# Kernel optimization log

Hardware: AMD Instinct MI355X
Metric: run time of the kernel (lower is better)

## Reference

```python
import jax, jax.numpy as jnp
import numpy as np

# Geometry constants hardcoded in the torch module
B, H, W = 1, 256, 256
A, DC = 64, 1024            # n_views, det_count
NSAMP = 512                  # samples per ray for the line integral
DSRC, DDET, SPACING = 500.0, 500.0, 2.0
NPAD = 2048                  # fft padding (next pow2 >= 2*DC)
FEAT = 32


def _bilinear_image(img, px, py):
    """Bilinear sample img (B,H,W) at centered coords px,py (any shape). Zero outside."""
    b, hh, ww = img.shape
    cx = px + (ww - 1) / 2.0
    cy = py + (hh - 1) / 2.0
    x0 = jnp.floor(cx); y0 = jnp.floor(cy)
    fx = cx - x0; fy = cy - y0
    x0i = x0.astype(jnp.int32); y0i = y0.astype(jnp.int32)
    flat = img.reshape(b, -1)

    def gather(yi, xi):
        valid = (yi >= 0) & (yi < hh) & (xi >= 0) & (xi < ww)
        yc = jnp.clip(yi, 0, hh - 1); xc = jnp.clip(xi, 0, ww - 1)
        idx = (yc * ww + xc).reshape(-1)
        v = jnp.take(flat, idx, axis=1).reshape((b,) + yi.shape)
        return v * valid.astype(img.dtype)

    return (gather(y0i, x0i) * (1 - fx) * (1 - fy)
            + gather(y0i, x0i + 1) * fx * (1 - fy)
            + gather(y0i + 1, x0i) * (1 - fx) * fy
            + gather(y0i + 1, x0i + 1) * fx * fy)


def fan_forward(img, theta):
    """Ray-driven fan-beam forward projection. img (B,1,H,W) -> sino (B,A,DC)."""
    im = img[:, 0]
    c = jnp.cos(theta); s = jnp.sin(theta)
    src = DSRC * jnp.stack([c, s], -1)                    # (A,2) source positions
    e = jnp.stack([-s, c], -1)                            # detector axis
    u = (jnp.arange(DC) - (DC - 1) / 2.0) * SPACING       # detector offsets
    det = -DDET * jnp.stack([c, s], -1)[:, None, :] + u[None, :, None] * e[:, None, :]  # (A,DC,2)
    d = det - src[:, None, :]
    L = jnp.sqrt(jnp.sum(d * d, axis=-1))                 # (A,DC) ray lengths
    t = (jnp.arange(NSAMP, dtype=jnp.float32) + 0.5) / NSAMP
    pts = src[:, None, None, :] + t[None, None, :, None] * d[:, :, None, :]  # (A,DC,N,2)
    vals = _bilinear_image(im, pts[..., 0], pts[..., 1])  # (B,A,DC,N)
    return jnp.sum(vals, axis=-1) * (L / NSAMP)[None]


def filter_sinogram(sino):
    """Ram-Lak ramp filtering along the detector axis with zero-padding."""
    f = jnp.abs(jnp.fft.rfftfreq(NPAD)).astype(jnp.float32)  # cycles/sample
    sf = jnp.fft.rfft(sino, n=NPAD, axis=-1) * (2.0 * f)
    return jnp.fft.irfft(sf, n=NPAD, axis=-1)[..., :DC].astype(sino.dtype)


def fan_backprojection(sino, theta):
    """Pixel-driven fan-beam backprojection. sino (B,A,DC) -> (B,1,H,W)."""
    xs = jnp.arange(W, dtype=jnp.float32) - (W - 1) / 2.0
    ys = jnp.arange(H, dtype=jnp.float32) - (H - 1) / 2.0
    gx, gy = jnp.meshgrid(xs, ys)                         # (H,W)
    c = jnp.cos(theta)[:, None, None]; s = jnp.sin(theta)[:, None, None]
    xr = gx[None] * c + gy[None] * s                      # (A,H,W) rotated coords
    yr = -gx[None] * s + gy[None] * c
    denom = DSRC - xr
    uu = yr * (DSRC + DDET) / denom                       # detector coordinate
    wgt = (DSRC * DSRC) / (denom * denom)                 # fan-beam distance weight
    iu = uu / SPACING + (DC - 1) / 2.0
    i0 = jnp.floor(iu); fr = iu - i0
    i0i = i0.astype(jnp.int32)
    aidx = jnp.arange(A)[:, None, None]
    b = sino.shape[0]
    flat = sino.reshape(b, -1)

    def g(ii):
        valid = (ii >= 0) & (ii < DC)
        ic = jnp.clip(ii, 0, DC - 1)
        idx = (aidx * DC + ic).reshape(-1)
        v = jnp.take(flat, idx, axis=1).reshape((b, A, H, W))
        return v * valid.astype(sino.dtype)

    vals = g(i0i) * (1 - fr) + g(i0i + 1) * fr            # (B,A,H,W)
    bp = jnp.sum(vals * wgt[None], axis=1) * (jnp.pi / A)
    return bp[:, None]


def conv(x, w):
    return jax.lax.conv_general_dilated(x, w, (1, 1), 'SAME',
                                        dimension_numbers=('NCHW', 'OIHW', 'NCHW'))


def setup_inputs():
    key = jax.random.key(0)
    ks = jax.random.split(key, 8)
    x = jax.random.normal(ks[0], (B, 1, H, W), jnp.float32)
    theta = jnp.arange(A, dtype=jnp.float32) * (2.0 * np.pi / A)
    sinogram = jax.random.normal(ks[1], (B, A, DC), jnp.float32)

    def xav(k, shape):
        fan_in = shape[1] * 9; fan_out = shape[0] * 9
        return jax.random.normal(k, shape, jnp.float32) * np.sqrt(2.0 / (fan_in + fan_out)).astype(np.float32)

    return {
        'x': x, 'theta': theta, 'sinogram': sinogram,
        'lambda_step': jnp.float32(0.5), 'soft_thr': jnp.float32(0.01),
        'conv1_forward': xav(ks[2], (FEAT, 1, 3, 3)),
        'conv2_forward': xav(ks[3], (FEAT, FEAT, 3, 3)),
        'conv1_backward': xav(ks[4], (FEAT, FEAT, 3, 3)),
        'conv2_backward': xav(ks[5], (1, FEAT, 3, 3)),
    }


def reference(x, theta, sinogram, lambda_step, soft_thr,
              conv1_forward, conv2_forward, conv1_backward, conv2_backward):
    sino_pred = fan_forward(x, theta)
    filtered = filter_sinogram(sino_pred)
    X_fbp = fan_backprojection(filtered - sinogram, theta)
    x_input = x - lambda_step * X_fbp
    h = jax.nn.relu(conv(x_input, conv1_forward))
    x_forward = conv(h, conv2_forward)
    hs = jnp.sign(x_forward) * jax.nn.relu(jnp.abs(x_forward) - soft_thr)
    x_pred = conv(jax.nn.relu(conv(hs, conv1_backward)), conv2_backward)
    x_est = conv(jax.nn.relu(conv(x_forward, conv1_backward)), conv2_backward)
    symloss = x_est - x_input
    return (x_pred, symloss)
```

## Files before the change

### kernel.cpp

```cpp
#include <hip/hip_runtime.h>

#define DEV_INLINE __device__ __forceinline__

#define PI_F 3.14159265358979323846f

#define H_OFF     0
#define SINO_OFF  2048
#define DIFF_OFF  67584
#define XIN_OFF   133120
#define WF2F_OFF  198656
#define WF1B_OFF  207872
#define WF2B_OFF  212480
#define BUFA_OFF  217088
#define BUFB_OFF  2314240

typedef short bf16x8 __attribute__((ext_vector_type(8)));
typedef float f32x4 __attribute__((ext_vector_type(4)));

union FragI4 { int4 i4; bf16x8 v; };
union I4U    { int4 i4; int i[4]; };

DEV_INLINE unsigned rne1(float a) {
  unsigned u = __float_as_uint(a);
  return (u + 0x7FFFu + ((u >> 16) & 1u)) >> 16;
}
DEV_INLINE int pack_rne(float a, float b) {
  return (int)(rne1(a) | (rne1(b) << 16));
}

__global__ __launch_bounds__(256) void setup_kernel(
    const float* __restrict__ sino_in, const float* __restrict__ w2f,
    const float* __restrict__ w1b, const float* __restrict__ w2b,
    const float* __restrict__ img,
    float* __restrict__ h, float* __restrict__ diff,
    int* __restrict__ wf2f, int* __restrict__ wf1b, int* __restrict__ wf2b,
    float4* __restrict__ quadP, float* __restrict__ x_input) {
  const int b = blockIdx.x;
  const int tid = threadIdx.x;
  if (b < 64) {
    __shared__ float hp[8][32];
    const int cell = tid & 31;
    const int kq = tid >> 5;
    const int n = b * 32 + cell;
    float ssum = 0.0f;
    const float ang_scale = PI_F / 1024.0f;
    for (int k = kq * 128; k < kq * 128 + 128; ++k) {
      int m = (k * n) & 2047;
      ssum += (float)k * __cosf((float)m * ang_scale);
    }
    hp[kq][cell] = ssum;
    __syncthreads();
    if (tid < 32) {
      float S = 0.0f;
      #pragma unroll
      for (int q = 0; q < 8; ++q) S += hp[q][tid];
      int nn = b * 32 + tid;
      float sgn = (nn & 1) ? -1.0f : 1.0f;
      h[nn] = (S * (1.0f / 512.0f) + sgn) * (1.0f / 2048.0f);
    }
  } else if (b < 320) {
    int idx = (b - 64) * 256 + tid;
    diff[idx] = -sino_in[idx];
  } else if (b < 356) {
    const bool second = (b >= 338);
    int idx = (b - (second ? 338 : 320)) * 256 + tid;
    int d = idx & 3;
    int L = (idx >> 2) & 63;
    int jm = idx >> 8;
    int j = jm >> 1, mt = jm & 1;
    int co = mt * 16 + (L & 15);
    int ci0 = (L >> 4) * 8 + 2 * d;
    const float* w = second ? w1b : w2f;
    int v = pack_rne(w[co * 288 + ci0 * 9 + j], w[co * 288 + (ci0 + 1) * 9 + j]);
    (second ? wf1b : wf2f)[idx] = v;
  } else if (b < 617) {
    int idx = (b - 356) * 256 + tid;
    if (idx < 258 * 258) {
      int y = idx / 258;
      int x = idx - y * 258;
      float4 v;
      int ay = y - 1, bx = x - 1;
      bool y0ok = (ay >= 0 && ay < 256);
      bool y1ok = (ay + 1 >= 0 && ay + 1 < 256);
      bool x0ok = (bx >= 0 && bx < 256);
      bool x1ok = (bx + 1 >= 0 && bx + 1 < 256);
      v.x = (y0ok && x0ok) ? img[(ay << 8) + bx] : 0.0f;
      v.y = (y0ok && x1ok) ? img[(ay << 8) + bx + 1] : 0.0f;
      v.z = (y1ok && x0ok) ? img[((ay + 1) << 8) + bx] : 0.0f;
      v.w = (y1ok && x1ok) ? img[((ay + 1) << 8) + bx + 1] : 0.0f;
      quadP[idx] = v;
    }
  } else if (b < 873) {
    int idx = (b - 617) * 256 + tid;
    x_input[idx] = img[idx];
  } else {
    int d = tid & 3;
    int L = tid >> 2;
    int n = L & 15;
    int k0 = (L >> 4) * 8 + 2 * d;
    float lo = (n < 9) ? w2b[k0 * 9 + n] : 0.0f;
    float hi = (n < 9) ? w2b[(k0 + 1) * 9 + n] : 0.0f;
    wf2b[tid] = pack_rne(lo, hi);
  }
}

__global__ __launch_bounds__(256) void fwdproj(
    const float4* __restrict__ quadP, const float* __restrict__ theta,
    float* __restrict__ sino) {
  __shared__ float part[8][32];
  __shared__ float cs[2];
  const int tid = threadIdx.x;
  const int a = blockIdx.x >> 5;
  const int cell = tid & 31;
  const int chunk = tid >> 5;
  const int d = ((blockIdx.x & 31) << 5) + cell;
  if (tid == 0) {
    float th = theta[a];
    cs[0] = cosf(th);
    cs[1] = sinf(th);
  }
  __syncthreads();
  const float c = cs[0], s = cs[1];
  const float u = ((float)d - 511.5f) * 2.0f;
  const float dxv = -1000.0f * c - u * s;
  const float dyv = -1000.0f * s + u * c;
  const float L = sqrtf(1.0e6f + u * u);
  const float sx = fmaf(500.0f, c, 127.5f);
  const float sy = fmaf(500.0f, s, 127.5f);

  float tlo = 0.0f, thi = 1.0f;
  if (fabsf(dxv) > 1e-6f) {
    float inv = 1.0f / dxv;
    float a0 = (-1.0f - sx) * inv, a1 = (256.0f - sx) * inv;
    tlo = fmaxf(tlo, fminf(a0, a1));
    thi = fminf(thi, fmaxf(a0, a1));
  } else if (sx <= -1.0f || sx >= 256.0f) {
    thi = -1.0f;
  }
  if (fabsf(dyv) > 1e-6f) {
    float inv = 1.0f / dyv;
    float a0 = (-1.0f - sy) * inv, a1 = (256.0f - sy) * inv;
    tlo = fmaxf(tlo, fminf(a0, a1));
    thi = fminf(thi, fmaxf(a0, a1));
  } else if (sy <= -1.0f || sy >= 256.0f) {
    thi = -1.0f;
  }
  int imin = (int)ceilf(tlo * 512.0f - 0.5f) - 1;
  imin = imin < 0 ? 0 : imin;
  int imax = (int)floorf(thi * 512.0f - 0.5f) + 1;
  imax = imax > 511 ? 511 : imax;

  float acc = 0.0f;
  for (int i = imin + chunk; i <= imax; i += 8) {
    float t = ((float)i + 0.5f) * (1.0f / 512.0f);
    float cx = fmaf(t, dxv, sx);
    float cy = fmaf(t, dyv, sy);
    cx = fminf(fmaxf(cx, -1.0f), 256.0f);
    cy = fminf(fmaxf(cy, -1.0f), 256.0f);
    float xf = floorf(cx), yf = floorf(cy);
    float fx = cx - xf, fy = cy - yf;
    int ix = (int)xf + 1;
    int iy = (int)yf + 1;
    float4 q = quadP[iy * 258 + ix];
    float gx = 1.0f - fx, gy = 1.0f - fy;
    acc += gy * (gx * q.x + fx * q.y) + fy * (gx * q.z + fx * q.w);
  }
  part[chunk][cell] = acc;
  __syncthreads();
  if (tid < 32) {
    float r = 0.0f;
    #pragma unroll
    for (int q = 0; q < 8; ++q) r += part[q][tid];
    sino[a * 1024 + ((blockIdx.x & 31) << 5) + tid] = r * (L * (1.0f / 512.0f));
  }
}

__global__ __launch_bounds__(256) void filt(
    const float* __restrict__ sino_pred, const float* __restrict__ h,
    float* __restrict__ diff) {
  __shared__ __align__(16) float srow[256];
  __shared__ __align__(16) float hext[4104];
  const int a = blockIdx.x >> 2;
  const int q = blockIdx.x & 3;
  const int tid = threadIdx.x;
  const int k0base = q * 256;
  srow[tid] = sino_pred[a * 1024 + k0base + tid];
  for (int n = tid; n < 4104; n += 256) hext[n] = h[(n - 2051) & 2047];
  __syncthreads();
  const int dd0 = tid * 4;
  float acc0 = 0.f, acc1 = 0.f, acc2 = 0.f, acc3 = 0.f;
  #pragma unroll 4
  for (int kk = 0; kk < 256; kk += 4) {
    float4 sv = *reinterpret_cast<const float4*>(&srow[kk]);
    int nb = dd0 + 2048 - k0base - kk;
    float4 hA = *reinterpret_cast<const float4*>(&hext[nb]);
    float4 hB = *reinterpret_cast<const float4*>(&hext[nb + 4]);
    acc0 = fmaf(sv.x, hA.w, acc0); acc0 = fmaf(sv.y, hA.z, acc0);
    acc0 = fmaf(sv.z, hA.y, acc0); acc0 = fmaf(sv.w, hA.x, acc0);
    acc1 = fmaf(sv.x, hB.x, acc1); acc1 = fmaf(sv.y, hA.w, acc1);
    acc1 = fmaf(sv.z, hA.z, acc1); acc1 = fmaf(sv.w, hA.y, acc1);
    acc2 = fmaf(sv.x, hB.y, acc2); acc2 = fmaf(sv.y, hB.x, acc2);
    acc2 = fmaf(sv.z, hA.w, acc2); acc2 = fmaf(sv.w, hA.z, acc2);
    acc3 = fmaf(sv.x, hB.z, acc3); acc3 = fmaf(sv.y, hB.y, acc3);
    acc3 = fmaf(sv.z, hB.x, acc3); acc3 = fmaf(sv.w, hA.w, acc3);
  }
  float* o = diff + a * 1024 + dd0;
  atomicAdd(o + 0, acc0);
  atomicAdd(o + 1, acc1);
  atomicAdd(o + 2, acc2);
  atomicAdd(o + 3, acc3);
}

__global__ __launch_bounds__(256) void backproj_part(
    const float* __restrict__ diff, const float* __restrict__ theta,
    const float* __restrict__ lam_p, float* __restrict__ x_input) {
  __shared__ float cst[16], snt[16];
  const int tid = threadIdx.x;
  const int tileb = blockIdx.x & 255;
  const int a0 = (blockIdx.x >> 8) << 4;
  if (tid < 16) {
    float th = theta[a0 + tid];
    cst[tid] = cosf(th);
    snt[tid] = sinf(th);
  }
  __syncthreads();
  const int tX = (tileb & 3) << 6;
  const int tY = (tileb >> 2) << 2;
  const int pxi = tX + (tid & 63);
  const int pyi = tY + (tid >> 6);
  const float gx = (float)pxi - 127.5f;
  const float gy = (float)pyi - 127.5f;
  float acc = 0.0f;
  for (int ai = 0; ai < 16; ++ai) {
    float c = cst[ai], s = snt[ai];
    float xr = gx * c + gy * s;
    float yr = gy * c - gx * s;
    float denom = 500.0f - xr;
    float inv = 1.0f / denom;
    float uu = yr * 1000.0f * inv;
    float wgt = 250000.0f * inv * inv;
    float iu = uu * 0.5f + 511.5f;
    float i0f = floorf(iu);
    float fr = iu - i0f;
    int i0 = (int)i0f;
    int c0 = min(max(i0, 0), 1023);
    int c1 = min(max(i0 + 1, 0), 1023);
    float m0 = (i0 >= 0 && i0 < 1024) ? 1.0f : 0.0f;
    float m1 = (i0 + 1 >= 0 && i0 + 1 < 1024) ? 1.0f : 0.0f;
    const float* row = diff + (a0 + ai) * 1024;
    float v0 = row[c0] * m0;
    float v1 = row[c1] * m1;
    acc += (v0 * (1.0f - fr) + v1 * fr) * wgt;
  }
  int p = (pyi << 8) + pxi;
  atomicAdd(x_input + p, -lam_p[0] * 0.04908738521234052f * acc);
}

__global__ __launch_bounds__(256) void conv12f(
    const float* __restrict__ x_input, const float* __restrict__ w1f,
    const int* __restrict__ wf2f, int* __restrict__ xfp) {
  __shared__ float xin[8][36];
  __shared__ __align__(16) int htile[3264];
  const int tid = threadIdx.x;
  const int lane = tid & 63;
  const int wave = tid >> 6;
  const int tX = (blockIdx.x & 7) << 5;
  const int tY = (blockIdx.x >> 3) << 2;

  FragI4 wf[2][9];
  const int4* wfg = (const int4*)wf2f;
  #pragma unroll
  for (int mt = 0; mt < 2; ++mt)
    #pragma unroll
    for (int j = 0; j < 9; ++j) wf[mt][j].i4 = wfg[(j * 2 + mt) * 64 + lane];

  for (int idx = tid; idx < 288; idx += 256) {
    int sy = idx / 36;
    int sx = idx - sy * 36;
    int gy = tY + sy - 2, gx = tX + sx - 2;
    xin[sy][sx] = (gy >= 0 && gy < 256 && gx >= 0 && gx < 256)
                      ? x_input[(gy << 8) + gx] : 0.0f;
  }
  __syncthreads();

  for (int pos = tid; pos < 204; pos += 256) {
    int yy = pos / 34;
    int xx = pos - yy * 34;
    int hy = tY + yy - 1, hx = tX + xx - 1;
    bool hin = (hy >= 0 && hy < 256 && hx >= 0 && hx < 256);
    float v[9];
    #pragma unroll
    for (int dy = 0; dy < 3; ++dy)
      #pragma unroll
      for (int dx = 0; dx < 3; ++dx) v[dy * 3 + dx] = xin[yy + dy][xx + dx];
    int packs[16];
    #pragma unroll
    for (int c2 = 0; c2 < 16; ++c2) {
      float r0 = 0.0f, r1 = 0.0f;
      #pragma unroll
      for (int j = 0; j < 9; ++j) {
        r0 = fmaf(v[j], w1f[(2 * c2) * 9 + j], r0);
        r1 = fmaf(v[j], w1f[(2 * c2 + 1) * 9 + j], r1);
      }
      r0 = hin ? fmaxf(r0, 0.0f) : 0.0f;
      r1 = hin ? fmaxf(r1, 0.0f) : 0.0f;
      packs[c2] = pack_rne(r0, r1);
    }
    #pragma unroll
    for (int g = 0; g < 4; ++g)
      *reinterpret_cast<int4*>(&htile[g * 816 + pos * 4]) =
          make_int4(packs[4 * g], packs[4 * g + 1],
                    packs[4 * g + 2], packs[4 * g + 3]);
  }
  __syncthreads();

  const int y = wave;
  const int n = lane & 15;
  const int q = lane >> 4;
  const int qb = q * 816;
  for (int xt = 0; xt < 2; ++xt) {
    const int x0 = xt << 4;
    f32x4 acc0 = {0.f, 0.f, 0.f, 0.f};
    f32x4 acc1 = {0.f, 0.f, 0.f, 0.f};
    #pragma unroll
    for (int j = 0; j < 9; ++j) {
      int dy = j / 3, dx = j - dy * 3;
      int pb = (y + dy) * 34 + x0 + dx + n;
      FragI4 bf;
      bf.i4 = *reinterpret_cast<const int4*>(&htile[qb + pb * 4]);
      acc0 = __builtin_amdgcn_mfma_f32_16x16x32_bf16(wf[0][j].v, bf.v, acc0, 0, 0, 0);
      acc1 = __builtin_amdgcn_mfma_f32_16x16x32_bf16(wf[1][j].v, bf.v, acc1, 0, 0, 0);
    }
    const int gpos = ((tY + y) << 8) + tX + x0 + n;
    int2* xp = (int2*)(xfp + (gpos << 4));
    xp[q]     = make_int2(pack_rne(acc0[0], acc0[1]), pack_rne(acc0[2], acc0[3]));
    xp[4 + q] = make_int2(pack_rne(acc1[0], acc1[1]), pack_rne(acc1[2], acc1[3]));
  }
}

__global__ __launch_bounds__(256) void branch_tail(
    const int* __restrict__ xfp, const int* __restrict__ wf1b,
    const int* __restrict__ wf2b, const float* __restrict__ thr_p,
    const float* __restrict__ x_input, float* __restrict__ out) {
  __shared__ __align__(16) int ldsX[8704];
  __shared__ __align__(16) int ldsD[6400];
  float* ldsP = (float*)ldsX;
  const int tid = threadIdx.x;
  const int lane = tid & 63;
  const int wave = tid >> 6;
  const int branch = blockIdx.x >> 8;
  const int tileb = blockIdx.x & 255;
  const int tX = (tileb & 3) << 6;
  const int tY = (tileb >> 2) << 2;
  const float thr = thr_p[0];
  const bool soft = (branch == 0);

  FragI4 wf[2][9];
  const int4* wfg = (const int4*)wf1b;
  #pragma unroll
  for (int mt = 0; mt < 2; ++mt)
    #pragma unroll
    for (int j = 0; j < 9; ++j) wf[mt][j].i4 = wfg[(j * 2 + mt) * 64 + lane];
  FragI4 wb;
  wb.i4 = ((const int4*)wf2b)[lane];

  if (tid < 16) {
    int g = tid >> 2, px = 396 + (tid & 3);
    *reinterpret_cast<int4*>(&ldsD[g * 1600 + px * 4]) = make_int4(0, 0, 0, 0);
  }

  #pragma unroll
  for (int t = 0; t < 3; ++t) {
    int p = tid + t * 256;
    if (p < 544) {
      int sy = p / 68;
      int sx = p - sy * 68;
      int gy = tY + sy - 2, gx = tX + sx - 2;
      bool ok = ((unsigned)gy < 256u) && ((unsigned)gx < 256u);
      I4U w[4];
      if (ok) {
        const int4* src = (const int4*)(xfp + (((gy << 8) + gx) << 4));
        w[0].i4 = src[0]; w[1].i4 = src[1]; w[2].i4 = src[2]; w[3].i4 = src[3];
      } else {
        w[0].i4 = w[1].i4 = w[2].i4 = w[3].i4 = make_int4(0, 0, 0, 0);
      }
      #pragma unroll
      for (int g = 0; g < 4; ++g) {
        if (soft) {
          #pragma unroll
          for (int k = 0; k < 4; ++k) {
            int v = w[g].i[k];
            float lo = __uint_as_float(((unsigned)v) << 16);
            float hi = __uint_as_float(((unsigned)v) & 0xFFFF0000u);
            lo = fmaxf(lo - thr, 0.0f) + fminf(lo + thr, 0.0f);
            hi = fmaxf(hi - thr, 0.0f) + fminf(hi + thr, 0.0f);
            w[g].i[k] = pack_rne(lo, hi);
          }
        }
        *reinterpret_cast<int4*>(&ldsX[g * 2176 + p * 4]) = w[g].i4;
      }
    }
  }
  __syncthreads();

  const int n = lane & 15;
  const int q = lane >> 4;
  const int rxtab[5] = {-1, 15, 31, 47, 49};
  for (int t = wave; t < 30; t += 4) {
    int trow = t / 5;
    int ry = trow - 1;
    int rx0 = rxtab[t - trow * 5];
    int rxn = rx0 + n;
    bool inimg = ((unsigned)(tX + rxn) < 256u) && ((unsigned)(tY + ry) < 256u);
    int pxD = (ry + 1) * 66 + rxn + 1;
    f32x4 acc0 = {0.f, 0.f, 0.f, 0.f};
    f32x4 acc1 = {0.f, 0.f, 0.f, 0.f};
    #pragma unroll
    for (int j = 0; j < 9; ++j) {
      int dy = j / 3, dx = j - dy * 3;
      int pb = (ry + 1 + dy) * 68 + rx0 + 1 + dx + n;
      FragI4 bf;
      bf.i4 = *reinterpret_cast<const int4*>(&ldsX[q * 2176 + pb * 4]);
      acc0 = __builtin_amdgcn_mfma_f32_16x16x32_bf16(wf[0][j].v, bf.v, acc0, 0, 0, 0);
      acc1 = __builtin_amdgcn_mfma_f32_16x16x32_bf16(wf[1][j].v, bf.v, acc1, 0, 0, 0);
    }
    float a00 = inimg ? fmaxf(acc0[0], 0.0f) : 0.0f;
    float a01 = inimg ? fmaxf(acc0[1], 0.0f) : 0.0f;
    float a02 = inimg ? fmaxf(acc0[2], 0.0f) : 0.0f;
    float a03 = inimg ? fmaxf(acc0[3], 0.0f) : 0.0f;
    float a10 = inimg ? fmaxf(acc1[0], 0.0f) : 0.0f;
    float a11 = inimg ? fmaxf(acc1[1], 0.0f) : 0.0f;
    float a12 = inimg ? fmaxf(acc1[2], 0.0f) : 0.0f;
    float a13 = inimg ? fmaxf(acc1[3], 0.0f) : 0.0f;
    *reinterpret_cast<int2*>(
        &ldsD[(q >> 1) * 1600 + pxD * 4 + (q & 1) * 2]) =
        make_int2(pack_rne(a00, a01), pack_rne(a02, a03));
    *reinterpret_cast<int2*>(
        &ldsD[(2 + (q >> 1)) * 1600 + pxD * 4 + (q & 1) * 2]) =
        make_int2(pack_rne(a10, a11), pack_rne(a12, a13));
  }
  __syncthreads();

  for (int t = wave; t < 25; t += 4) {
    int pbase = t << 4;
    FragI4 af;
    af.i4 = *reinterpret_cast<const int4*>(&ldsD[q * 1600 + (pbase + n) * 4]);
    f32x4 acc = {0.f, 0.f, 0.f, 0.f};
    acc = __builtin_amdgcn_mfma_f32_16x16x32_bf16(af.v, wb.v, acc, 0, 0, 0);
    #pragma unroll
    for (int r = 0; r < 4; ++r)
      ldsP[(pbase + q * 4 + r) * 17 + n] = acc[r];
  }
  __syncthreads();

  const int px = tid & 63, py = tid >> 6;
  float acc = 0.0f;
  #pragma unroll
  for (int j = 0; j < 9; ++j) {
    int dy = j / 3, dx = j - dy * 3;
    int rp = (py + dy) * 66 + px + dx;
    acc += ldsP[rp * 17 + j];
  }
  const int p = ((tY + py) << 8) + tX + px;
  if (branch == 0) out[p] = acc;
  else out[65536 + p] = acc - x_input[p];
}

extern "C" void kernel_launch(void* const* d_in, const int* in_sizes, int n_in,
                              void* d_out, int out_size, void* d_ws, size_t ws_size,
                              hipStream_t stream) {
  const float* x       = (const float*)d_in[0];
  const float* theta   = (const float*)d_in[1];
  const float* sino_in = (const float*)d_in[2];
  const float* lam     = (const float*)d_in[3];
  const float* thr     = (const float*)d_in[4];
  const float* w_c1f   = (const float*)d_in[5];
  const float* w_c2f   = (const float*)d_in[6];
  const float* w_c1b   = (const float*)d_in[7];
  const float* w_c2b   = (const float*)d_in[8];
  float* out = (float*)d_out;
  float* ws  = (float*)d_ws;

  float* h         = ws + H_OFF;
  float* sino_pred = ws + SINO_OFF;
  float* diff      = ws + DIFF_OFF;
  float* x_input   = ws + XIN_OFF;
  int*   wf2f      = (int*)(ws + WF2F_OFF);
  int*   wf1b      = (int*)(ws + WF1B_OFF);
  int*   wf2b      = (int*)(ws + WF2B_OFF);
  float4* quadP    = (float4*)(ws + BUFA_OFF);
  int*   xfp       = (int*)(ws + BUFB_OFF);

  setup_kernel<<<874, 256, 0, stream>>>(sino_in, w_c2f, w_c1b, w_c2b, x, h,
                                        diff, wf2f, wf1b, wf2b, quadP, x_input);
  fwdproj<<<2048, 256, 0, stream>>>(quadP, theta, sino_pred);
  filt<<<256, 256, 0, stream>>>(sino_pred, h, diff);
  backproj_part<<<1024, 256, 0, stream>>>(diff, theta, lam, x_input);
  conv12f<<<512, 256, 0, stream>>>(x_input, w_c1f, wf2f, xfp);
  branch_tail<<<512, 256, 0, stream>>>(xfp, wf1b, wf2b, thr, x_input, out);
}
```

Measured before the change: 127.4 us.

## Fuse forward projection into setup kernel and reduce backprojection in-block

Drops the padded quad-image precompute. The forward projector now samples the raw image directly, with per-tap bounds-masked weights, and runs in the same launch as the setup work, which removes one kernel launch and one dependency. Backprojection gives each block all 64 angles split over four thread groups, reduces them in shared memory, and writes x_input = img - lambda*sum directly. That replaces the atomic accumulation and the separate x_input copy. In exchange, each bilinear sample now issues four scalar loads instead of one float4 load.

```diff
diff --git a/kernel.cpp b/kernel.cpp
--- a/kernel.cpp
+++ b/kernel.cpp
@@ -11,7 +11,6 @@
 #define WF2F_OFF  198656
 #define WF1B_OFF  207872
 #define WF2B_OFF  212480
-#define BUFA_OFF  217088
 #define BUFB_OFF  2314240
 
 typedef short bf16x8 __attribute__((ext_vector_type(8)));
@@ -28,20 +27,98 @@
   return (int)(rne1(a) | (rne1(b) << 16));
 }
 
-__global__ __launch_bounds__(256) void setup_kernel(
-    const float* __restrict__ sino_in, const float* __restrict__ w2f,
-    const float* __restrict__ w1b, const float* __restrict__ w2b,
-    const float* __restrict__ img,
+__global__ __launch_bounds__(256) void k1_fwd_setup(
+    const float* __restrict__ img, const float* __restrict__ theta,
+    const float* __restrict__ sino_in,
+    const float* __restrict__ w2f, const float* __restrict__ w1b,
+    const float* __restrict__ w2b,
     float* __restrict__ h, float* __restrict__ diff,
     int* __restrict__ wf2f, int* __restrict__ wf1b, int* __restrict__ wf2b,
-    float4* __restrict__ quadP, float* __restrict__ x_input) {
+    float* __restrict__ sino) {
   const int b = blockIdx.x;
   const int tid = threadIdx.x;
-  if (b < 64) {
+  if (b < 2048) {
+    __shared__ float part[8][32];
+    __shared__ float cs[2];
+    const int a = b >> 5;
+    const int cell = tid & 31;
+    const int chunk = tid >> 5;
+    const int d = ((b & 31) << 5) + cell;
+    if (tid == 0) {
+      float th = theta[a];
+      cs[0] = cosf(th);
+      cs[1] = sinf(th);
+    }
+    __syncthreads();
+    const float c = cs[0], s = cs[1];
+    const float u = ((float)d - 511.5f) * 2.0f;
+    const float dxv = -1000.0f * c - u * s;
+    const float dyv = -1000.0f * s + u * c;
+    const float L = sqrtf(1.0e6f + u * u);
+    const float sx = fmaf(500.0f, c, 127.5f);
+    const float sy = fmaf(500.0f, s, 127.5f);
+
+    float tlo = 0.0f, thi = 1.0f;
+    if (fabsf(dxv) > 1e-6f) {
+      float inv = 1.0f / dxv;
+      float a0 = (-1.0f - sx) * inv, a1 = (256.0f - sx) * inv;
+      tlo = fmaxf(tlo, fminf(a0, a1));
+      thi = fminf(thi, fmaxf(a0, a1));
+    } else if (sx <= -1.0f || sx >= 256.0f) {
+      thi = -1.0f;
+    }
+    if (fabsf(dyv) > 1e-6f) {
+      float inv = 1.0f / dyv;
+      float a0 = (-1.0f - sy) * inv, a1 = (256.0f - sy) * inv;
+      tlo = fmaxf(tlo, fminf(a0, a1));
+      thi = fminf(thi, fmaxf(a0, a1));
+    } else if (sy <= -1.0f || sy >= 256.0f) {
+      thi = -1.0f;
+    }
+    int imin = (int)ceilf(tlo * 512.0f - 0.5f) - 1;
+    imin = imin < 0 ? 0 : imin;
+    int imax = (int)floorf(thi * 512.0f - 0.5f) + 1;
+    imax = imax > 511 ? 511 : imax;
+
+    float acc = 0.0f;
+    for (int i = imin + chunk; i <= imax; i += 8) {
+      float t = ((float)i + 0.5f) * (1.0f / 512.0f);
+      float cx = fmaf(t, dxv, sx);
+      float cy = fmaf(t, dyv, sy);
+      cx = fminf(fmaxf(cx, -1.0f), 256.0f);
+      cy = fminf(fmaxf(cy, -1.0f), 256.0f);
+      float xf = floorf(cx), yf = floorf(cy);
+      float fx = cx - xf, fy = cy - yf;
+      int ix = (int)xf;
+      int iy = (int)yf;
+      float wx0 = ((unsigned)ix < 256u) ? (1.0f - fx) : 0.0f;
+      float wx1 = ((unsigned)(ix + 1) < 256u) ? fx : 0.0f;
+      float wy0 = ((unsigned)iy < 256u) ? (1.0f - fy) : 0.0f;
+      float wy1 = ((unsigned)(iy + 1) < 256u) ? fy : 0.0f;
+      int ix0 = min(max(ix, 0), 255);
+      int ix1 = min(ix + 1, 255);
+      int iy0 = min(max(iy, 0), 255);
+      int iy1 = min(iy + 1, 255);
+      const float* r0 = img + (iy0 << 8);
+      const float* r1 = img + (iy1 << 8);
+      float h0 = fmaf(wx1, r0[ix1], wx0 * r0[ix0]);
+      float h1 = fmaf(wx1, r1[ix1], wx0 * r1[ix0]);
+      acc = fmaf(wy0, h0, fmaf(wy1, h1, acc));
+    }
+    part[chunk][cell] = acc;
+    __syncthreads();
+    if (tid < 32) {
+      float r = 0.0f;
+      #pragma unroll
+      for (int q = 0; q < 8; ++q) r += part[q][tid];
+      sino[a * 1024 + ((b & 31) << 5) + tid] = r * (L * (1.0f / 512.0f));
+    }
+  } else if (b < 2112) {
     __shared__ float hp[8][32];
+    const int hb = b - 2048;
     const int cell = tid & 31;
     const int kq = tid >> 5;
-    const int n = b * 32 + cell;
+    const int n = hb * 32 + cell;
     float ssum = 0.0f;
     const float ang_scale = PI_F / 1024.0f;
     for (int k = kq * 128; k < kq * 128 + 128; ++k) {
@@ -54,16 +131,17 @@
       float S = 0.0f;
       #pragma unroll
       for (int q = 0; q < 8; ++q) S += hp[q][tid];
-      int nn = b * 32 + tid;
+      int nn = hb * 32 + tid;
       float sgn = (nn & 1) ? -1.0f : 1.0f;
       h[nn] = (S * (1.0f / 512.0f) + sgn) * (1.0f / 2048.0f);
     }
-  } else if (b < 320) {
-    int idx = (b - 64) * 256 + tid;
+  } else if (b < 2368) {
+    int idx = (b - 2112) * 256 + tid;
     diff[idx] = -sino_in[idx];
-  } else if (b < 356) {
-    const bool second = (b >= 338);
-    int idx = (b - (second ? 338 : 320)) * 256 + tid;
+  } else if (b < 2404) {
+    const int bb = b - 2368;
+    const bool second = (bb >= 18);
+    int idx = (second ? bb - 18 : bb) * 256 + tid;
     int d = idx & 3;
     int L = (idx >> 2) & 63;
     int jm = idx >> 8;
@@ -73,26 +151,6 @@
     const float* w = second ? w1b : w2f;
     int v = pack_rne(w[co * 288 + ci0 * 9 + j], w[co * 288 + (ci0 + 1) * 9 + j]);
     (second ? wf1b : wf2f)[idx] = v;
-  } else if (b < 617) {
-    int idx = (b - 356) * 256 + tid;
-    if (idx < 258 * 258) {
-      int y = idx / 258;
-      int x = idx - y * 258;
-      float4 v;
-      int ay = y - 1, bx = x - 1;
-      bool y0ok = (ay >= 0 && ay < 256);
-      bool y1ok = (ay + 1 >= 0 && ay + 1 < 256);
-      bool x0ok = (bx >= 0 && bx < 256);
-      bool x1ok = (bx + 1 >= 0 && bx + 1 < 256);
-      v.x = (y0ok && x0ok) ? img[(ay << 8) + bx] : 0.0f;
-      v.y = (y0ok && x1ok) ? img[(ay << 8) + bx + 1] : 0.0f;
-      v.z = (y1ok && x0ok) ? img[((ay + 1) << 8) + bx] : 0.0f;
-      v.w = (y1ok && x1ok) ? img[((ay + 1) << 8) + bx + 1] : 0.0f;
-      quadP[idx] = v;
-    }
-  } else if (b < 873) {
-    int idx = (b - 617) * 256 + tid;
-    x_input[idx] = img[idx];
   } else {
     int d = tid & 3;
     int L = tid >> 2;
@@ -101,77 +159,6 @@
     float lo = (n < 9) ? w2b[k0 * 9 + n] : 0.0f;
     float hi = (n < 9) ? w2b[(k0 + 1) * 9 + n] : 0.0f;
     wf2b[tid] = pack_rne(lo, hi);
-  }
-}
-
-__global__ __launch_bounds__(256) void fwdproj(
-    const float4* __restrict__ quadP, const float* __restrict__ theta,
-    float* __restrict__ sino) {
-  __shared__ float part[8][32];
-  __shared__ float cs[2];
-  const int tid = threadIdx.x;
-  const int a = blockIdx.x >> 5;
-  const int cell = tid & 31;
-  const int chunk = tid >> 5;
-  const int d = ((blockIdx.x & 31) << 5) + cell;
-  if (tid == 0) {
-    float th = theta[a];
-    cs[0] = cosf(th);
-    cs[1] = sinf(th);
-  }
-  __syncthreads();
-  const float c = cs[0], s = cs[1];
-  const float u = ((float)d - 511.5f) * 2.0f;
-  const float dxv = -1000.0f * c - u * s;
-  const float dyv = -1000.0f * s + u * c;
-  const float L = sqrtf(1.0e6f + u * u);
-  const float sx = fmaf(500.0f, c, 127.5f);
-  const float sy = fmaf(500.0f, s, 127.5f);
-
-  float tlo = 0.0f, thi = 1.0f;
-  if (fabsf(dxv) > 1e-6f) {
-    float inv = 1.0f / dxv;
-    float a0 = (-1.0f - sx) * inv, a1 = (256.0f - sx) * inv;
-    tlo = fmaxf(tlo, fminf(a0, a1));
-    thi = fminf(thi, fmaxf(a0, a1));
-  } else if (sx <= -1.0f || sx >= 256.0f) {
-    thi = -1.0f;
-  }
-  if (fabsf(dyv) > 1e-6f) {
-    float inv = 1.0f / dyv;
-    float a0 = (-1.0f - sy) * inv, a1 = (256.0f - sy) * inv;
-    tlo = fmaxf(tlo, fminf(a0, a1));
-    thi = fminf(thi, fmaxf(a0, a1));
-  } else if (sy <= -1.0f || sy >= 256.0f) {
-    thi = -1.0f;
-  }
-  int imin = (int)ceilf(tlo * 512.0f - 0.5f) - 1;
-  imin = imin < 0 ? 0 : imin;
-  int imax = (int)floorf(thi * 512.0f - 0.5f) + 1;
-  imax = imax > 511 ? 511 : imax;
-
-  float acc = 0.0f;
-  for (int i = imin + chunk; i <= imax; i += 8) {
-    float t = ((float)i + 0.5f) * (1.0f / 512.0f);
-    float cx = fmaf(t, dxv, sx);
-    float cy = fmaf(t, dyv, sy);
-    cx = fminf(fmaxf(cx, -1.0f), 256.0f);
-    cy = fminf(fmaxf(cy, -1.0f), 256.0f);
-    float xf = floorf(cx), yf = floorf(cy);
-    float fx = cx - xf, fy = cy - yf;
-    int ix = (int)xf + 1;
-    int iy = (int)yf + 1;
-    float4 q = quadP[iy * 258 + ix];
-    float gx = 1.0f - fx, gy = 1.0f - fy;
-    acc += gy * (gx * q.x + fx * q.y) + fy * (gx * q.z + fx * q.w);
-  }
-  part[chunk][cell] = acc;
-  __syncthreads();
-  if (tid < 32) {
-    float r = 0.0f;
-    #pragma unroll
-    for (int q = 0; q < 8; ++q) r += part[q][tid];
-    sino[a * 1024 + ((blockIdx.x & 31) << 5) + tid] = r * (L * (1.0f / 512.0f));
   }
 }
 
@@ -211,27 +198,29 @@
   atomicAdd(o + 3, acc3);
 }
 
-__global__ __launch_bounds__(256) void backproj_part(
+__global__ __launch_bounds__(512) void backproj(
     const float* __restrict__ diff, const float* __restrict__ theta,
-    const float* __restrict__ lam_p, float* __restrict__ x_input) {
-  __shared__ float cst[16], snt[16];
+    const float* __restrict__ lam_p, const float* __restrict__ img,
+    float* __restrict__ x_input) {
+  __shared__ float cst[64], snt[64];
+  __shared__ float part[512];
   const int tid = threadIdx.x;
-  const int tileb = blockIdx.x & 255;
-  const int a0 = (blockIdx.x >> 8) << 4;
-  if (tid < 16) {
-    float th = theta[a0 + tid];
+  if (tid < 64) {
+    float th = theta[tid];
     cst[tid] = cosf(th);
     snt[tid] = sinf(th);
   }
   __syncthreads();
-  const int tX = (tileb & 3) << 6;
-  const int tY = (tileb >> 2) << 2;
-  const int pxi = tX + (tid & 63);
-  const int pyi = tY + (tid >> 6);
+  const int tX = (blockIdx.x & 7) << 5;
+  const int tY = (blockIdx.x >> 3) << 2;
+  const int pl = tid & 127;
+  const int ag = tid >> 7;
+  const int pxi = tX + (pl & 31);
+  const int pyi = tY + (pl >> 5);
   const float gx = (float)pxi - 127.5f;
   const float gy = (float)pyi - 127.5f;
   float acc = 0.0f;
-  for (int ai = 0; ai < 16; ++ai) {
+  for (int ai = ag * 16; ai < ag * 16 + 16; ++ai) {
     float c = cst[ai], s = snt[ai];
     float xr = gx * c + gy * s;
     float yr = gy * c - gx * s;
@@ -247,13 +236,18 @@
     int c1 = min(max(i0 + 1, 0), 1023);
     float m0 = (i0 >= 0 && i0 < 1024) ? 1.0f : 0.0f;
     float m1 = (i0 + 1 >= 0 && i0 + 1 < 1024) ? 1.0f : 0.0f;
-    const float* row = diff + (a0 + ai) * 1024;
+    const float* row = diff + ai * 1024;
     float v0 = row[c0] * m0;
     float v1 = row[c1] * m1;
     acc += (v0 * (1.0f - fr) + v1 * fr) * wgt;
   }
-  int p = (pyi << 8) + pxi;
-  atomicAdd(x_input + p, -lam_p[0] * 0.04908738521234052f * acc);
+  part[tid] = acc;
+  __syncthreads();
+  if (tid < 128) {
+    float sum = part[tid] + part[tid + 128] + part[tid + 256] + part[tid + 384];
+    int p = ((tY + (tid >> 5)) << 8) + tX + (tid & 31);
+    x_input[p] = img[p] - lam_p[0] * 0.04908738521234052f * sum;
+  }
 }
 
 __global__ __launch_bounds__(256) void conv12f(
@@ -488,14 +482,13 @@
   int*   wf2f      = (int*)(ws + WF2F_OFF);
   int*   wf1b      = (int*)(ws + WF1B_OFF);
   int*   wf2b      = (int*)(ws + WF2B_OFF);
-  float4* quadP    = (float4*)(ws + BUFA_OFF);
   int*   xfp       = (int*)(ws + BUFB_OFF);
 
-  setup_kernel<<<874, 256, 0, stream>>>(sino_in, w_c2f, w_c1b, w_c2b, x, h,
-                                        diff, wf2f, wf1b, wf2b, quadP, x_input);
-  fwdproj<<<2048, 256, 0, stream>>>(quadP, theta, sino_pred);
+  k1_fwd_setup<<<2405, 256, 0, stream>>>(x, theta, sino_in, w_c2f, w_c1b,
+                                         w_c2b, h, diff, wf2f, wf1b, wf2b,
+                                         sino_pred);
   filt<<<256, 256, 0, stream>>>(sino_pred, h, diff);
-  backproj_part<<<1024, 256, 0, stream>>>(diff, theta, lam, x_input);
+  backproj<<<512, 512, 0, stream>>>(diff, theta, lam, x, x_input);
   conv12f<<<512, 256, 0, stream>>>(x_input, w_c1f, wf2f, xfp);
   branch_tail<<<512, 256, 0, stream>>>(xfp, wf1b, wf2b, thr, x_input, out);
 }
```

Result: slower. 146.6 us (+15.0%).

## Reduce backprojection in-block, drop x_input copy, unroll forward projection gathers

Applied to the files above, without the earlier changes.

The backprojection now reduces all 64 views inside one 512-thread block through shared memory. It writes x_input = img - lambda*sum directly, which removes the global float atomics and the setup pass that copied img into x_input. The forward projector changes to 64 detector cells by 4 sample chunks per block and issues four independent quadP gathers per iteration, with masks on the tail samples, to raise memory-level parallelism. Fewer, larger blocks may reduce occupancy or load balance.

```diff
diff --git a/kernel.cpp b/kernel.cpp
--- a/kernel.cpp
+++ b/kernel.cpp
@@ -34,7 +34,7 @@
     const float* __restrict__ img,
     float* __restrict__ h, float* __restrict__ diff,
     int* __restrict__ wf2f, int* __restrict__ wf1b, int* __restrict__ wf2b,
-    float4* __restrict__ quadP, float* __restrict__ x_input) {
+    float4* __restrict__ quadP) {
   const int b = blockIdx.x;
   const int tid = threadIdx.x;
   if (b < 64) {
@@ -90,9 +90,6 @@
       v.w = (y1ok && x1ok) ? img[((ay + 1) << 8) + bx + 1] : 0.0f;
       quadP[idx] = v;
     }
-  } else if (b < 873) {
-    int idx = (b - 617) * 256 + tid;
-    x_input[idx] = img[idx];
   } else {
     int d = tid & 3;
     int L = tid >> 2;
@@ -107,13 +104,13 @@
 __global__ __launch_bounds__(256) void fwdproj(
     const float4* __restrict__ quadP, const float* __restrict__ theta,
     float* __restrict__ sino) {
-  __shared__ float part[8][32];
+  __shared__ float part[4][64];
   __shared__ float cs[2];
   const int tid = threadIdx.x;
-  const int a = blockIdx.x >> 5;
-  const int cell = tid & 31;
-  const int chunk = tid >> 5;
-  const int d = ((blockIdx.x & 31) << 5) + cell;
+  const int a = blockIdx.x >> 4;
+  const int cell = tid & 63;
+  const int chunk = tid >> 6;
+  const int d = ((blockIdx.x & 15) << 6) + cell;
   if (tid == 0) {
     float th = theta[a];
     cs[0] = cosf(th);
@@ -124,7 +121,6 @@
   const float u = ((float)d - 511.5f) * 2.0f;
   const float dxv = -1000.0f * c - u * s;
   const float dyv = -1000.0f * s + u * c;
-  const float L = sqrtf(1.0e6f + u * u);
   const float sx = fmaf(500.0f, c, 127.5f);
   const float sy = fmaf(500.0f, s, 127.5f);
 
@@ -151,27 +147,56 @@
   imax = imax > 511 ? 511 : imax;
 
   float acc = 0.0f;
-  for (int i = imin + chunk; i <= imax; i += 8) {
-    float t = ((float)i + 0.5f) * (1.0f / 512.0f);
-    float cx = fmaf(t, dxv, sx);
-    float cy = fmaf(t, dyv, sy);
-    cx = fminf(fmaxf(cx, -1.0f), 256.0f);
-    cy = fminf(fmaxf(cy, -1.0f), 256.0f);
-    float xf = floorf(cx), yf = floorf(cy);
-    float fx = cx - xf, fy = cy - yf;
-    int ix = (int)xf + 1;
-    int iy = (int)yf + 1;
-    float4 q = quadP[iy * 258 + ix];
-    float gx = 1.0f - fx, gy = 1.0f - fy;
-    acc += gy * (gx * q.x + fx * q.y) + fy * (gx * q.z + fx * q.w);
+  for (int i = imin + chunk; i <= imax; i += 16) {
+    int idxs[4];
+    float fxs[4], fys[4];
+    #pragma unroll
+    for (int k = 0; k < 4; ++k) {
+      float t = ((float)(i + 4 * k) + 0.5f) * (1.0f / 512.0f);
+      float cx = fmaf(t, dxv, sx);
+      float cy = fmaf(t, dyv, sy);
+      cx = fminf(fmaxf(cx, -1.0f), 256.0f);
+      cy = fminf(fmaxf(cy, -1.0f), 256.0f);
+      float xf = floorf(cx), yf = floorf(cy);
+      fxs[k] = cx - xf;
+      fys[k] = cy - yf;
+      idxs[k] = ((int)yf + 1) * 258 + (int)xf + 1;
+    }
+    float4 q0 = quadP[idxs[0]];
+    float4 q1 = quadP[idxs[1]];
+    float4 q2 = quadP[idxs[2]];
+    float4 q3 = quadP[idxs[3]];
+    {
+      float gx = 1.0f - fxs[0], gy = 1.0f - fys[0];
+      acc += gy * (gx * q0.x + fxs[0] * q0.y) + fys[0] * (gx * q0.z + fxs[0] * q0.w);
+    }
+    {
+      float m = (i + 4 <= imax) ? 1.0f : 0.0f;
+      float gx = 1.0f - fxs[1], gy = 1.0f - fys[1];
+      float cv = gy * (gx * q1.x + fxs[1] * q1.y) + fys[1] * (gx * q1.z + fxs[1] * q1.w);
+      acc = fmaf(m, cv, acc);
+    }
+    {
+      float m = (i + 8 <= imax) ? 1.0f : 0.0f;
+      float gx = 1.0f - fxs[2], gy = 1.0f - fys[2];
+      float cv = gy * (gx * q2.x + fxs[2] * q2.y) + fys[2] * (gx * q2.z + fxs[2] * q2.w);
+      acc = fmaf(m, cv, acc);
+    }
+    {
+      float m = (i + 12 <= imax) ? 1.0f : 0.0f;
+      float gx = 1.0f - fxs[3], gy = 1.0f - fys[3];
+      float cv = gy * (gx * q3.x + fxs[3] * q3.y) + fys[3] * (gx * q3.z + fxs[3] * q3.w);
+      acc = fmaf(m, cv, acc);
+    }
   }
   part[chunk][cell] = acc;
   __syncthreads();
-  if (tid < 32) {
-    float r = 0.0f;
-    #pragma unroll
-    for (int q = 0; q < 8; ++q) r += part[q][tid];
-    sino[a * 1024 + ((blockIdx.x & 31) << 5) + tid] = r * (L * (1.0f / 512.0f));
+  if (tid < 64) {
+    float r = part[0][tid] + part[1][tid] + part[2][tid] + part[3][tid];
+    int dr = ((blockIdx.x & 15) << 6) + tid;
+    float ur = ((float)dr - 511.5f) * 2.0f;
+    float Lr = sqrtf(1.0e6f + ur * ur);
+    sino[a * 1024 + dr] = r * (Lr * (1.0f / 512.0f));
   }
 }
 
@@ -211,27 +236,29 @@
   atomicAdd(o + 3, acc3);
 }
 
-__global__ __launch_bounds__(256) void backproj_part(
+__global__ __launch_bounds__(512) void backproj(
     const float* __restrict__ diff, const float* __restrict__ theta,
-    const float* __restrict__ lam_p, float* __restrict__ x_input) {
-  __shared__ float cst[16], snt[16];
+    const float* __restrict__ lam_p, const float* __restrict__ img,
+    float* __restrict__ x_input) {
+  __shared__ float cst[64], snt[64];
+  __shared__ float part[512];
   const int tid = threadIdx.x;
-  const int tileb = blockIdx.x & 255;
-  const int a0 = (blockIdx.x >> 8) << 4;
-  if (tid < 16) {
-    float th = theta[a0 + tid];
+  if (tid < 64) {
+    float th = theta[tid];
     cst[tid] = cosf(th);
     snt[tid] = sinf(th);
   }
   __syncthreads();
-  const int tX = (tileb & 3) << 6;
-  const int tY = (tileb >> 2) << 2;
-  const int pxi = tX + (tid & 63);
-  const int pyi = tY + (tid >> 6);
+  const int tX = (blockIdx.x & 7) << 5;
+  const int tY = (blockIdx.x >> 3) << 2;
+  const int pl = tid & 127;
+  const int ag = tid >> 7;
+  const int pxi = tX + (pl & 31);
+  const int pyi = tY + (pl >> 5);
   const float gx = (float)pxi - 127.5f;
   const float gy = (float)pyi - 127.5f;
   float acc = 0.0f;
-  for (int ai = 0; ai < 16; ++ai) {
+  for (int ai = ag * 16; ai < ag * 16 + 16; ++ai) {
     float c = cst[ai], s = snt[ai];
     float xr = gx * c + gy * s;
     float yr = gy * c - gx * s;
@@ -247,13 +274,18 @@
     int c1 = min(max(i0 + 1, 0), 1023);
     float m0 = (i0 >= 0 && i0 < 1024) ? 1.0f : 0.0f;
     float m1 = (i0 + 1 >= 0 && i0 + 1 < 1024) ? 1.0f : 0.0f;
-    const float* row = diff + (a0 + ai) * 1024;
+    const float* row = diff + ai * 1024;
     float v0 = row[c0] * m0;
     float v1 = row[c1] * m1;
     acc += (v0 * (1.0f - fr) + v1 * fr) * wgt;
   }
-  int p = (pyi << 8) + pxi;
-  atomicAdd(x_input + p, -lam_p[0] * 0.04908738521234052f * acc);
+  part[tid] = acc;
+  __syncthreads();
+  if (tid < 128) {
+    float sum = part[tid] + part[tid + 128] + part[tid + 256] + part[tid + 384];
+    int p = ((tY + (tid >> 5)) << 8) + tX + (tid & 31);
+    x_input[p] = img[p] - lam_p[0] * 0.04908738521234052f * sum;
+  }
 }
 
 __global__ __launch_bounds__(256) void conv12f(
@@ -491,11 +523,11 @@
   float4* quadP    = (float4*)(ws + BUFA_OFF);
   int*   xfp       = (int*)(ws + BUFB_OFF);
 
-  setup_kernel<<<874, 256, 0, stream>>>(sino_in, w_c2f, w_c1b, w_c2b, x, h,
-                                        diff, wf2f, wf1b, wf2b, quadP, x_input);
-  fwdproj<<<2048, 256, 0, stream>>>(quadP, theta, sino_pred);
+  setup_kernel<<<618, 256, 0, stream>>>(sino_in, w_c2f, w_c1b, w_c2b, x, h,
+                                        diff, wf2f, wf1b, wf2b, quadP);
+  fwdproj<<<1024, 256, 0, stream>>>(quadP, theta, sino_pred);
   filt<<<256, 256, 0, stream>>>(sino_pred, h, diff);
-  backproj_part<<<1024, 256, 0, stream>>>(diff, theta, lam, x_input);
+  backproj<<<512, 512, 0, stream>>>(diff, theta, lam, x, x_input);
   conv12f<<<512, 256, 0, stream>>>(x_input, w_c1f, wf2f, xfp);
   branch_tail<<<512, 256, 0, stream>>>(xfp, wf1b, wf2b, thr, x_input, out);
 }
```

New measurement: 131.4 us. +3.1%, slower.
